# Kernel tuning notes

Measured on AMD Instinct MI355X. Metric: run time of the kernel, lower is better.

Reference implementation:

```python
import jax, jax.numpy as jnp
import numpy as np

M_DIM = 32          # vec_dim m
L1 = L2 = L3 = L4 = 3
L_TOT = L1 * L2 * L3 * L4   # 81
R = 2               # rank1..rank4 window size
B_SZ = 4
D_SZ = 16           # D1 = D2 = D3 = D4


def _make_bbasis():
    # Bbasis[idx, i] = prod_k cos(2*pi*(j_k+1)/(i+2)), idx = flattened (j1,j2,j3,j4)
    i = jnp.arange(M_DIM, dtype=jnp.float32)
    def c(Lk):
        j = jnp.arange(Lk, dtype=jnp.float32)
        return jnp.cos(2.0 * jnp.pi * (j[:, None] + 1.0) / (i[None, :] + 2.0))  # [Lk, m]
    c1, c2, c3, c4 = c(L1), c(L2), c(L3), c(L4)
    Bb = (c1[:, None, None, None, :] * c2[None, :, None, None, :]
          * c3[None, None, :, None, :] * c4[None, None, None, :, :])
    return Bb.reshape(L_TOT, M_DIM)


def _window_basis_idx(n1, n2, n3, n4):
    # linear mode, drop: window top-left coords are 0..n_k-1 with step 1
    j1 = jnp.arange(n1) % L1
    j2 = jnp.arange(n2) % L2
    j3 = jnp.arange(n3) % L3
    j4 = jnp.arange(n4) % L4
    idx = (((j1[:, None, None, None] * L2 + j2[None, :, None, None]) * L3
            + j3[None, None, :, None]) * L4 + j4[None, None, None, :])
    return idx.reshape(-1)  # [n_windows]


def setup_inputs() -> dict:
    key = jax.random.key(0)
    k1, k2, k3 = jax.random.split(key, 3)
    arr_batch = jax.random.normal(k1, (B_SZ, D_SZ, D_SZ, D_SZ, D_SZ, M_DIM), dtype=jnp.float32)
    # M initialized near identity (nn.init.eye_ + perturbation so grads are non-trivial)
    M = jnp.eye(M_DIM, dtype=jnp.float32) + 0.01 * jax.random.normal(k2, (M_DIM, M_DIM), dtype=jnp.float32)
    # Acoeff ~ U(-0.1, 0.1) as in reset_parameters
    Acoeff = jax.random.uniform(k3, (M_DIM, L_TOT), dtype=jnp.float32, minval=-0.1, maxval=0.1)
    Bbasis = _make_bbasis()  # fixed buffer, computed deterministically
    return {"arr_batch": arr_batch, "M": M, "Acoeff": Acoeff, "Bbasis": Bbasis}


def reference(arr_batch, M, Acoeff, Bbasis):
    Bsz, D1, D2, D3, D4, m = arr_batch.shape
    # map every vector through M (x @ M.T); avg-pooling commutes with the linear map,
    # matching `mapped = windows @ M.T` then mean over the window
    mapped = jnp.einsum('bpqrsm,nm->bpqrsn', arr_batch, M)
    # 4D sliding window (rank=2 per dim, stride 1, 'drop' -> VALID), rank_op='avg'
    win = (1, R, R, R, R, 1)
    agg = jax.lax.reduce_window(mapped, 0.0, jax.lax.add, win, (1,) * 6, 'VALID') / float(R ** 4)
    n1, n2, n3, n4 = agg.shape[1:5]
    n_win = n1 * n2 * n3 * n4
    agg = agg.reshape(Bsz, n_win, m)            # [B, W, m]
    idx = _window_basis_idx(n1, n2, n3, n4)     # [W]
    phi = Bbasis[idx]                           # [W, m]
    # t_k = Acoeff[:, j_k] * (Bbasis[j_k, :] . agg_k); representation = mean_k t_k
    s = jnp.einsum('bwm,wm->bw', agg, phi)      # [B, W]
    t = s[:, :, None] * Acoeff.T[idx][None]     # [B, W, m]
    return t.mean(axis=1)                       # [B, m]
```

## Files before the change

kernel.cpp:

```cpp
#include <hip/hip_runtime.h>


static __device__ __forceinline__ void add4(float4& a, const float4& b) {
    a.x += b.x; a.y += b.y; a.z += b.z; a.w += b.w;
}
static __device__ __forceinline__ void fma4(float4& a, float w, const float4& b) {
    a.x = fmaf(w, b.x, a.x); a.y = fmaf(w, b.y, a.y);
    a.z = fmaf(w, b.z, a.z); a.w = fmaf(w, b.w, a.w);
}

__global__ __launch_bounds__(128) void sdd4_fused(
    const float* __restrict__ arr,
    const float* __restrict__ Mmat,
    const float* __restrict__ Bbasis,
    const float* __restrict__ Acoeff,
    float* __restrict__ out)
{
    __shared__ float4 U_lds[400];
    __shared__ float  V_lds[9 * 33];
    __shared__ float  Y_lds[9 * 33];
    __shared__ float  M_lds[32 * 33];
    __shared__ float  B_lds[81 * 33];
    __shared__ float  pv[36];
    __shared__ int    jfv[36];

    const int t  = threadIdx.x;
    const int bx = blockIdx.x;
    const int b  = bx >> 8;
    const int p  = (bx >> 4) & 15;
    const int q  = bx & 15;

    const float4* M4 = reinterpret_cast<const float4*>(Mmat);
    for (int i = t; i < 256; i += 128) {
        float4 v = M4[i];
        float* dst = &M_lds[(i >> 3) * 33 + (i & 7) * 4];
        dst[0] = v.x; dst[1] = v.y; dst[2] = v.z; dst[3] = v.w;
    }
    const float4* B4 = reinterpret_cast<const float4*>(Bbasis);
    for (int i = t; i < 648; i += 128) {
        float4 v = B4[i];
        float* dst = &B_lds[(i >> 3) * 33 + (i & 7) * 4];
        dst[0] = v.x; dst[1] = v.y; dst[2] = v.z; dst[3] = v.w;
    }

    const int r  = t >> 3;
    const int mv = t & 7;
    const float4* A4 = reinterpret_cast<const float4*>(arr);
    const size_t tile = (size_t)((b * 16 + p) * 16 + q) * 2048;

    float4 u0 = make_float4(0.f, 0.f, 0.f, 0.f), u1 = u0, u2 = u0;
    #pragma unroll
    for (int s = 0; s < 16; ++s) {
        float4 x = A4[tile + (size_t)(r * 16 + s) * 8 + mv];
        if ((0x36DBu >> s) & 1) add4(u0, x);
        if ((0x6DB6u >> s) & 1) add4(u1, x);
        if ((0xDB6Cu >> s) & 1) add4(u2, x);
    }
    U_lds[r * 25 +      mv] = u0;
    U_lds[r * 25 +  8 + mv] = u1;
    U_lds[r * 25 + 16 + mv] = u2;
    __syncthreads();

    if (t < 72) {
        const int j3  = t / 24;
        const int rem = t % 24;
        const int j4  = rem >> 3;
        const int mv2 = rem & 7;
        const unsigned msk = (j3 == 0) ? 0x36DBu : (j3 == 1 ? 0x6DB6u : 0xDB6Cu);
        float4 acc = make_float4(0.f, 0.f, 0.f, 0.f);
        #pragma unroll
        for (int rr = 0; rr < 16; ++rr) {
            float w = (float)((msk >> rr) & 1u);
            fma4(acc, w, U_lds[rr * 25 + j4 * 8 + mv2]);
        }
        const int jj = j3 * 3 + j4;
        float* dv = &V_lds[jj * 33 + mv2 * 4];
        dv[0] = acc.x; dv[1] = acc.y; dv[2] = acc.z; dv[3] = acc.w;
    }
    __syncthreads();

    for (int o = t; o < 288; o += 128) {
        const int jj = o >> 5;
        const int n  = o & 31;
        float acc = 0.f;
        #pragma unroll
        for (int m = 0; m < 32; ++m)
            acc = fmaf(M_lds[n * 33 + m], V_lds[jj * 33 + m], acc);
        Y_lds[jj * 33 + n] = acc;
    }
    __syncthreads();

    int l1_0, l1_1 = 0, n1;
    if      (p == 0)  { l1_0 = 0; n1 = 1; }
    else if (p == 15) { l1_0 = 2; n1 = 1; }
    else              { l1_0 = (p - 1) % 3; l1_1 = p % 3; n1 = 2; }
    int l2_0, l2_1 = 0, n2;
    if      (q == 0)  { l2_0 = 0; n2 = 1; }
    else if (q == 15) { l2_0 = 2; n2 = 1; }
    else              { l2_0 = (q - 1) % 3; l2_1 = q % 3; n2 = 2; }

    const int ncomb = n1 * n2 * 9;
    if (t < ncomb) {
        const int jj  = t % 9;
        const int c12 = t / 9;
        const int i1idx = (n2 == 2) ? (c12 >> 1) : c12;
        const int i2idx = (n2 == 2) ? (c12 & 1)  : 0;
        const int i1 = i1idx ? l1_1 : l1_0;
        const int i2 = i2idx ? l2_1 : l2_0;
        const int jf = (i1 * 3 + i2) * 9 + jj;
        float acc = 0.f;
        #pragma unroll
        for (int n = 0; n < 32; ++n)
            acc = fmaf(Y_lds[jj * 33 + n], B_lds[jf * 33 + n], acc);
        pv[t]  = acc;
        jfv[t] = jf;
    }
    __syncthreads();

    if (t < 32) {
        float acc = 0.f;
        for (int c = 0; c < ncomb; ++c)
            acc = fmaf(Acoeff[t * 81 + jfv[c]], pv[c], acc);
        atomicAdd(&out[b * 32 + t], acc * (1.0f / 810000.0f));
    }
}

extern "C" void kernel_launch(void* const* d_in, const int* in_sizes, int n_in,
                              void* d_out, int out_size, void* d_ws, size_t ws_size,
                              hipStream_t stream) {
    const float* arr    = (const float*)d_in[0];
    const float* Mmat   = (const float*)d_in[1];
    const float* Acoeff = (const float*)d_in[2];
    const float* Bbasis = (const float*)d_in[3];

    hipMemsetAsync(d_out, 0, 4 * 32 * sizeof(float), stream);
    sdd4_fused<<<dim3(1024), dim3(128), 0, stream>>>(arr, Mmat, Bbasis, Acoeff,
                                                     (float*)d_out);
}
```

Before: 88.42 us.

## Precompute Bbasis·M in a prologue kernel and drop the per-block M matmul

Adds a small prologue kernel that computes BM = Bbasis @ M once and zeroes the output, which replaces the hipMemsetAsync. The main kernel then dots the pooled vectors directly with BM rows, removing the per-block 9x32x32 M-multiply stage and one barrier. Acoeff is also staged into LDS, and the final loop runs a fixed 36 iterations with masked-out combinations contributing zero. In exchange there is a second launch on the same stream, and each block now loads Acoeff into LDS and uses more shared memory, which may lower occupancy.

```diff
diff --git a/kernel.cpp b/kernel.cpp
--- a/kernel.cpp
+++ b/kernel.cpp
@@ -9,18 +9,37 @@
     a.z = fmaf(w, b.z, a.z); a.w = fmaf(w, b.w, a.w);
 }
 
+__global__ __launch_bounds__(64) void sdd4_bm(
+    const float* __restrict__ Mmat,
+    const float* __restrict__ Bbasis,
+    float* __restrict__ BM,
+    float* __restrict__ out)
+{
+    __shared__ float Bb_sh[32];
+    const int t = threadIdx.x;
+    const int j = blockIdx.x;
+    if (j == 0) { out[t] = 0.f; out[64 + t] = 0.f; }
+    if (t < 32) Bb_sh[t] = Bbasis[j * 32 + t];
+    __syncthreads();
+    if (t < 32) {
+        float acc = 0.f;
+        #pragma unroll
+        for (int n = 0; n < 32; ++n)
+            acc = fmaf(Bb_sh[n], Mmat[n * 32 + t], acc);
+        BM[j * 32 + t] = acc;
+    }
+}
+
 __global__ __launch_bounds__(128) void sdd4_fused(
     const float* __restrict__ arr,
-    const float* __restrict__ Mmat,
-    const float* __restrict__ Bbasis,
+    const float* __restrict__ BM,
     const float* __restrict__ Acoeff,
     float* __restrict__ out)
 {
     __shared__ float4 U_lds[400];
     __shared__ float  V_lds[9 * 33];
-    __shared__ float  Y_lds[9 * 33];
-    __shared__ float  M_lds[32 * 33];
-    __shared__ float  B_lds[81 * 33];
+    __shared__ float  BM_lds[81 * 33];
+    __shared__ float4 A_lds4[648];
     __shared__ float  pv[36];
     __shared__ int    jfv[36];
 
@@ -30,28 +49,25 @@
     const int p  = (bx >> 4) & 15;
     const int q  = bx & 15;
 
-    const float4* M4 = reinterpret_cast<const float4*>(Mmat);
-    for (int i = t; i < 256; i += 128) {
-        float4 v = M4[i];
-        float* dst = &M_lds[(i >> 3) * 33 + (i & 7) * 4];
+    const float4* BM4 = reinterpret_cast<const float4*>(BM);
+    for (int i = t; i < 648; i += 128) {
+        float4 v = BM4[i];
+        float* dst = &BM_lds[(i >> 3) * 33 + (i & 7) * 4];
         dst[0] = v.x; dst[1] = v.y; dst[2] = v.z; dst[3] = v.w;
     }
-    const float4* B4 = reinterpret_cast<const float4*>(Bbasis);
-    for (int i = t; i < 648; i += 128) {
-        float4 v = B4[i];
-        float* dst = &B_lds[(i >> 3) * 33 + (i & 7) * 4];
-        dst[0] = v.x; dst[1] = v.y; dst[2] = v.z; dst[3] = v.w;
-    }
+    const float4* A4 = reinterpret_cast<const float4*>(Acoeff);
+    for (int i = t; i < 648; i += 128) A_lds4[i] = A4[i];
+    const float* A_lds = reinterpret_cast<const float*>(A_lds4);
 
     const int r  = t >> 3;
     const int mv = t & 7;
-    const float4* A4 = reinterpret_cast<const float4*>(arr);
+    const float4* Ar4 = reinterpret_cast<const float4*>(arr);
     const size_t tile = (size_t)((b * 16 + p) * 16 + q) * 2048;
 
     float4 u0 = make_float4(0.f, 0.f, 0.f, 0.f), u1 = u0, u2 = u0;
     #pragma unroll
     for (int s = 0; s < 16; ++s) {
-        float4 x = A4[tile + (size_t)(r * 16 + s) * 8 + mv];
+        float4 x = Ar4[tile + (size_t)(r * 16 + s) * 8 + mv];
         if ((0x36DBu >> s) & 1) add4(u0, x);
         if ((0x6DB6u >> s) & 1) add4(u1, x);
         if ((0xDB6Cu >> s) & 1) add4(u2, x);
@@ -79,17 +95,6 @@
     }
     __syncthreads();
 
-    for (int o = t; o < 288; o += 128) {
-        const int jj = o >> 5;
-        const int n  = o & 31;
-        float acc = 0.f;
-        #pragma unroll
-        for (int m = 0; m < 32; ++m)
-            acc = fmaf(M_lds[n * 33 + m], V_lds[jj * 33 + m], acc);
-        Y_lds[jj * 33 + n] = acc;
-    }
-    __syncthreads();
-
     int l1_0, l1_1 = 0, n1;
     if      (p == 0)  { l1_0 = 0; n1 = 1; }
     else if (p == 15) { l1_0 = 2; n1 = 1; }
@@ -99,19 +104,21 @@
     else if (q == 15) { l2_0 = 2; n2 = 1; }
     else              { l2_0 = (q - 1) % 3; l2_1 = q % 3; n2 = 2; }
 
-    const int ncomb = n1 * n2 * 9;
-    if (t < ncomb) {
-        const int jj  = t % 9;
-        const int c12 = t / 9;
-        const int i1idx = (n2 == 2) ? (c12 >> 1) : c12;
-        const int i2idx = (n2 == 2) ? (c12 & 1)  : 0;
-        const int i1 = i1idx ? l1_1 : l1_0;
-        const int i2 = i2idx ? l2_1 : l2_0;
+    if (t < 36) {
+        const int jj   = t % 9;
+        const int c12  = t / 9;
+        const int asel = c12 >> 1;
+        const int bsel = c12 & 1;
+        const int i1 = asel ? l1_1 : l1_0;
+        const int i2 = bsel ? l2_1 : l2_0;
+        const bool ok = (!asel || n1 == 2) && (!bsel || n2 == 2);
         const int jf = (i1 * 3 + i2) * 9 + jj;
         float acc = 0.f;
-        #pragma unroll
-        for (int n = 0; n < 32; ++n)
-            acc = fmaf(Y_lds[jj * 33 + n], B_lds[jf * 33 + n], acc);
+        if (ok) {
+            #pragma unroll
+            for (int m = 0; m < 32; ++m)
+                acc = fmaf(V_lds[jj * 33 + m], BM_lds[jf * 33 + m], acc);
+        }
         pv[t]  = acc;
         jfv[t] = jf;
     }
@@ -119,8 +126,9 @@
 
     if (t < 32) {
         float acc = 0.f;
-        for (int c = 0; c < ncomb; ++c)
-            acc = fmaf(Acoeff[t * 81 + jfv[c]], pv[c], acc);
+        #pragma unroll
+        for (int c = 0; c < 36; ++c)
+            acc = fmaf(A_lds[t * 81 + jfv[c]], pv[c], acc);
         atomicAdd(&out[b * 32 + t], acc * (1.0f / 810000.0f));
     }
 }
@@ -132,8 +140,8 @@
     const float* Mmat   = (const float*)d_in[1];
     const float* Acoeff = (const float*)d_in[2];
     const float* Bbasis = (const float*)d_in[3];
+    float* BM = (float*)d_ws;
 
-    hipMemsetAsync(d_out, 0, 4 * 32 * sizeof(float), stream);
-    sdd4_fused<<<dim3(1024), dim3(128), 0, stream>>>(arr, Mmat, Bbasis, Acoeff,
-                                                     (float*)d_out);
+    sdd4_bm   <<<dim3(81),   dim3(64),  0, stream>>>(Mmat, Bbasis, BM, (float*)d_out);
+    sdd4_fused<<<dim3(1024), dim3(128), 0, stream>>>(arr, BM, Acoeff, (float*)d_out);
 }
```

Result: no change. 87.71 us (-0.8%).

## Split into stream-reduce kernel plus small grouped reduction over (b, j3j4)

Applied to the files above, without the earlier changes.

The fused kernel is split in two. The first pass reduces the input over the two inner window dimensions and writes per-(p,q) partial sums to workspace, with the output zeroed in-kernel instead of by a separate memset. A second 36-block kernel groups the (p,q) partials by residue class, then applies the M projection, the basis dot product and Acoeff once per group. This removes the per-block M/Bbasis loading and the per-block matvecs, at the cost of a workspace round trip and a second launch. Zeroing out in block 0 while other blocks never read it is safe here because only the second kernel accumulates into it.

```diff
diff --git a/kernel.cpp b/kernel.cpp
--- a/kernel.cpp
+++ b/kernel.cpp
@@ -9,20 +9,12 @@
     a.z = fmaf(w, b.z, a.z); a.w = fmaf(w, b.w, a.w);
 }
 
-__global__ __launch_bounds__(128) void sdd4_fused(
+__global__ __launch_bounds__(128) void sdd4_v(
     const float* __restrict__ arr,
-    const float* __restrict__ Mmat,
-    const float* __restrict__ Bbasis,
-    const float* __restrict__ Acoeff,
+    float* __restrict__ V,
     float* __restrict__ out)
 {
     __shared__ float4 U_lds[400];
-    __shared__ float  V_lds[9 * 33];
-    __shared__ float  Y_lds[9 * 33];
-    __shared__ float  M_lds[32 * 33];
-    __shared__ float  B_lds[81 * 33];
-    __shared__ float  pv[36];
-    __shared__ int    jfv[36];
 
     const int t  = threadIdx.x;
     const int bx = blockIdx.x;
@@ -30,18 +22,7 @@
     const int p  = (bx >> 4) & 15;
     const int q  = bx & 15;
 
-    const float4* M4 = reinterpret_cast<const float4*>(Mmat);
-    for (int i = t; i < 256; i += 128) {
-        float4 v = M4[i];
-        float* dst = &M_lds[(i >> 3) * 33 + (i & 7) * 4];
-        dst[0] = v.x; dst[1] = v.y; dst[2] = v.z; dst[3] = v.w;
-    }
-    const float4* B4 = reinterpret_cast<const float4*>(Bbasis);
-    for (int i = t; i < 648; i += 128) {
-        float4 v = B4[i];
-        float* dst = &B_lds[(i >> 3) * 33 + (i & 7) * 4];
-        dst[0] = v.x; dst[1] = v.y; dst[2] = v.z; dst[3] = v.w;
-    }
+    if (bx == 0) out[t] = 0.f;
 
     const int r  = t >> 3;
     const int mv = t & 7;
@@ -74,54 +55,103 @@
             fma4(acc, w, U_lds[rr * 25 + j4 * 8 + mv2]);
         }
         const int jj = j3 * 3 + j4;
-        float* dv = &V_lds[jj * 33 + mv2 * 4];
-        dv[0] = acc.x; dv[1] = acc.y; dv[2] = acc.z; dv[3] = acc.w;
+        float4* V4 = reinterpret_cast<float4*>(V);
+        V4[((b * 9 + jj) * 256 + p * 16 + q) * 8 + mv2] = acc;
+    }
+}
+
+__global__ __launch_bounds__(256) void sdd4_reduce(
+    const float* __restrict__ V,
+    const float* __restrict__ Mmat,
+    const float* __restrict__ Bbasis,
+    const float* __restrict__ Acoeff,
+    float* __restrict__ out)
+{
+    __shared__ float M_lds[32 * 33];
+    __shared__ float Bb_lds[9 * 33];
+    __shared__ float Vp[8 * 9 * 33];
+    __shared__ float Vs[9 * 33];
+    __shared__ float Y_lds[9 * 33];
+    __shared__ float Sf[9];
+
+    const int t   = threadIdx.x;
+    const int blk = blockIdx.x;
+    const int b   = blk / 9;
+    const int jj  = blk % 9;
+
+    const float4* M4 = reinterpret_cast<const float4*>(Mmat);
+    if (t < 256) {
+        float4 v = M4[t];
+        float* dst = &M_lds[(t >> 3) * 33 + (t & 7) * 4];
+        dst[0] = v.x; dst[1] = v.y; dst[2] = v.z; dst[3] = v.w;
+    }
+    const float4* B4 = reinterpret_cast<const float4*>(Bbasis);
+    if (t < 72) {
+        const int k = t >> 3, f4 = t & 7;
+        float4 v = B4[(k * 9 + jj) * 8 + f4];
+        float* dst = &Bb_lds[k * 33 + f4 * 4];
+        dst[0] = v.x; dst[1] = v.y; dst[2] = v.z; dst[3] = v.w;
+    }
+
+    const int g = t >> 5;
+    const int m = t & 31;
+    const float* Vb = V + (size_t)blk * 8192;
+    float acc[9];
+    #pragma unroll
+    for (int c = 0; c < 9; ++c) acc[c] = 0.f;
+    #pragma unroll 4
+    for (int u = 0; u < 32; ++u) {
+        const int pq = g * 32 + u;
+        const int p  = pq >> 4;
+        const int q  = pq & 15;
+        const float v = Vb[pq * 32 + m];
+        const unsigned e1 = ((0x36DBu >> p) & 1u) | (((0x6DB6u >> p) & 1u) << 1)
+                          | (((0xDB6Cu >> p) & 1u) << 2);
+        const unsigned e2 = ((0x36DBu >> q) & 1u) | (((0x6DB6u >> q) & 1u) << 1)
+                          | (((0xDB6Cu >> q) & 1u) << 2);
+        #pragma unroll
+        for (int c = 0; c < 9; ++c)
+            if (((e1 >> (c / 3)) & 1u) && ((e2 >> (c % 3)) & 1u))
+                acc[c] += v;
+    }
+    #pragma unroll
+    for (int c = 0; c < 9; ++c) Vp[(g * 9 + c) * 33 + m] = acc[c];
+    __syncthreads();
+
+    for (int o = t; o < 288; o += 256) {
+        const int c = o >> 5, mm = o & 31;
+        float s = 0.f;
+        #pragma unroll
+        for (int gg = 0; gg < 8; ++gg) s += Vp[(gg * 9 + c) * 33 + mm];
+        Vs[c * 33 + mm] = s;
     }
     __syncthreads();
 
-    for (int o = t; o < 288; o += 128) {
-        const int jj = o >> 5;
-        const int n  = o & 31;
-        float acc = 0.f;
+    for (int o = t; o < 288; o += 256) {
+        const int c = o >> 5, n = o & 31;
+        float s = 0.f;
         #pragma unroll
-        for (int m = 0; m < 32; ++m)
-            acc = fmaf(M_lds[n * 33 + m], V_lds[jj * 33 + m], acc);
-        Y_lds[jj * 33 + n] = acc;
+        for (int mm = 0; mm < 32; ++mm)
+            s = fmaf(M_lds[n * 33 + mm], Vs[c * 33 + mm], s);
+        Y_lds[c * 33 + n] = s;
     }
     __syncthreads();
 
-    int l1_0, l1_1 = 0, n1;
-    if      (p == 0)  { l1_0 = 0; n1 = 1; }
-    else if (p == 15) { l1_0 = 2; n1 = 1; }
-    else              { l1_0 = (p - 1) % 3; l1_1 = p % 3; n1 = 2; }
-    int l2_0, l2_1 = 0, n2;
-    if      (q == 0)  { l2_0 = 0; n2 = 1; }
-    else if (q == 15) { l2_0 = 2; n2 = 1; }
-    else              { l2_0 = (q - 1) % 3; l2_1 = q % 3; n2 = 2; }
-
-    const int ncomb = n1 * n2 * 9;
-    if (t < ncomb) {
-        const int jj  = t % 9;
-        const int c12 = t / 9;
-        const int i1idx = (n2 == 2) ? (c12 >> 1) : c12;
-        const int i2idx = (n2 == 2) ? (c12 & 1)  : 0;
-        const int i1 = i1idx ? l1_1 : l1_0;
-        const int i2 = i2idx ? l2_1 : l2_0;
-        const int jf = (i1 * 3 + i2) * 9 + jj;
-        float acc = 0.f;
+    if (t < 9) {
+        float s = 0.f;
         #pragma unroll
         for (int n = 0; n < 32; ++n)
-            acc = fmaf(Y_lds[jj * 33 + n], B_lds[jf * 33 + n], acc);
-        pv[t]  = acc;
-        jfv[t] = jf;
+            s = fmaf(Bb_lds[t * 33 + n], Y_lds[t * 33 + n], s);
+        Sf[t] = s;
     }
     __syncthreads();
 
     if (t < 32) {
-        float acc = 0.f;
-        for (int c = 0; c < ncomb; ++c)
-            acc = fmaf(Acoeff[t * 81 + jfv[c]], pv[c], acc);
-        atomicAdd(&out[b * 32 + t], acc * (1.0f / 810000.0f));
+        float z = 0.f;
+        #pragma unroll
+        for (int c = 0; c < 9; ++c)
+            z = fmaf(Acoeff[t * 81 + c * 9 + jj], Sf[c], z);
+        atomicAdd(&out[b * 32 + t], z * (1.0f / 810000.0f));
     }
 }
 
@@ -132,8 +162,9 @@
     const float* Mmat   = (const float*)d_in[1];
     const float* Acoeff = (const float*)d_in[2];
     const float* Bbasis = (const float*)d_in[3];
+    float* V = (float*)d_ws;
 
-    hipMemsetAsync(d_out, 0, 4 * 32 * sizeof(float), stream);
-    sdd4_fused<<<dim3(1024), dim3(128), 0, stream>>>(arr, Mmat, Bbasis, Acoeff,
-                                                     (float*)d_out);
+    sdd4_v     <<<dim3(1024), dim3(128), 0, stream>>>(arr, V, (float*)d_out);
+    sdd4_reduce<<<dim3(36),   dim3(256), 0, stream>>>(V, Mmat, Bbasis, Acoeff,
+                                                      (float*)d_out);
 }
```

Result: faster. 84.48 us (median of 2 runs) (-4.5%).
